# Kernel tuning notes

Measured on AMD Instinct MI355X. Metric: run time of the kernel, lower is better.

The kernel has to match this reference:

```python
import jax, jax.numpy as jnp
from jax import lax
import numpy as np

FEAT_STRIDE = 16
PRE_NMS_TOP_N = 2000
POST_NMS_TOP_N = 300
NMS_THRESH = 0.7


def _whctrs(a):
    w = a[2] - a[0] + 1.0
    h = a[3] - a[1] + 1.0
    return w, h, a[0] + 0.5 * (w - 1.0), a[1] + 0.5 * (h - 1.0)


def _mkanchors(ws, hs, x_ctr, y_ctr):
    ws = np.asarray(ws, dtype=np.float64)
    hs = np.asarray(hs, dtype=np.float64)
    return np.stack([x_ctr - 0.5 * (ws - 1.0), y_ctr - 0.5 * (hs - 1.0),
                     x_ctr + 0.5 * (ws - 1.0), y_ctr + 0.5 * (hs - 1.0)], axis=1)


def generate_anchors(base_size=16, ratios=np.array([0.5, 1.0, 2.0]), scales=np.array([8.0, 16.0, 32.0])):
    base = np.array([1.0, 1.0, float(base_size), float(base_size)]) - 1.0
    w, h, xc, yc = _whctrs(base)
    size = w * h
    ws = np.round(np.sqrt(size / ratios))
    hs = np.round(ws * ratios)
    ratio_anchors = _mkanchors(ws, hs, xc, yc)
    out = []
    for i in range(ratio_anchors.shape[0]):
        w_i, h_i, xc_i, yc_i = _whctrs(ratio_anchors[i])
        out.append(_mkanchors(w_i * scales, h_i * scales, xc_i, yc_i))
    return np.vstack(out).astype(np.float32)


ANCHORS = generate_anchors()  # [A=9, 4]
NUM_ANCHORS = ANCHORS.shape[0]


def _nms_keep(boxes, thresh):
    # boxes [N,4], already sorted by descending score; torchvision IoU convention.
    x1, y1, x2, y2 = boxes[:, 0], boxes[:, 1], boxes[:, 2], boxes[:, 3]
    areas = (x2 - x1) * (y2 - y1)
    xx1 = jnp.maximum(x1[:, None], x1[None, :])
    yy1 = jnp.maximum(y1[:, None], y1[None, :])
    xx2 = jnp.minimum(x2[:, None], x2[None, :])
    yy2 = jnp.minimum(y2[:, None], y2[None, :])
    inter = jnp.clip(xx2 - xx1, 0.0) * jnp.clip(yy2 - yy1, 0.0)
    iou = inter / (areas[:, None] + areas[None, :] - inter + 1e-9)
    n = boxes.shape[0]
    # sup[i, j] True => box i (higher score) suppresses later box j
    sup = (iou > thresh) & jnp.triu(jnp.ones((n, n), bool), 1)

    def body(i, keep):
        return keep & ~(keep[i] & sup[i])

    return lax.fori_loop(0, n, body, jnp.ones((n,), bool))


def setup_inputs() -> dict:
    key = jax.random.key(0)
    k1, k2 = jax.random.split(key)
    B, A, H, W = 8, NUM_ANCHORS, 128, 128
    scores = jax.random.normal(k1, (B, 2 * A, H, W), jnp.float32)
    bbox_deltas = jax.random.normal(k2, (B, 4 * A, H, W), jnp.float32) * 0.2
    im_h = float(H * FEAT_STRIDE)
    im_w = float(W * FEAT_STRIDE)
    im_info = jnp.tile(jnp.array([[im_h, im_w, 1.0]], jnp.float32), (B, 1))
    return {"scores": scores, "bbox_deltas": bbox_deltas, "im_info": im_info}


def reference(scores, bbox_deltas, im_info):
    B, _, H, W = scores.shape
    A = NUM_ANCHORS
    # --- anchor generation over the feature grid ---
    sx = jnp.arange(W, dtype=jnp.float32) * FEAT_STRIDE
    sy = jnp.arange(H, dtype=jnp.float32) * FEAT_STRIDE
    gx, gy = jnp.meshgrid(sx, sy)  # 'xy' indexing matches np.meshgrid default
    shifts = jnp.stack([gx.ravel(), gy.ravel(), gx.ravel(), gy.ravel()], axis=1)  # [K,4]
    anchors = (jnp.asarray(ANCHORS)[None, :, :] + shifts[:, None, :]).reshape(-1, 4)  # [K*A,4]

    obj_scores = scores[:, A:].transpose(0, 2, 3, 1).reshape(B, -1)   # [B, K*A]
    deltas = bbox_deltas.transpose(0, 2, 3, 1).reshape(B, -1, 4)      # [B, K*A, 4]

    # --- bbox_transform_inv ---
    widths = anchors[:, 2] - anchors[:, 0] + 1.0
    heights = anchors[:, 3] - anchors[:, 1] + 1.0
    ctr_x = anchors[:, 0] + 0.5 * widths
    ctr_y = anchors[:, 1] + 0.5 * heights
    dx, dy, dw, dh = deltas[..., 0], deltas[..., 1], deltas[..., 2], deltas[..., 3]
    pred_ctr_x = dx * widths + ctr_x
    pred_ctr_y = dy * heights + ctr_y
    pred_w = jnp.exp(dw) * widths
    pred_h = jnp.exp(dh) * heights
    proposals = jnp.stack([pred_ctr_x - 0.5 * pred_w, pred_ctr_y - 0.5 * pred_h,
                           pred_ctr_x + 0.5 * pred_w, pred_ctr_y + 0.5 * pred_h], axis=-1)

    # --- clip_boxes: im_info[b] = (h, w, scale) ---
    max_x = (im_info[:, 1] - 1.0)[:, None]
    max_y = (im_info[:, 0] - 1.0)[:, None]
    proposals = jnp.stack([
        jnp.clip(proposals[..., 0], 0.0, max_x),
        jnp.clip(proposals[..., 1], 0.0, max_y),
        jnp.clip(proposals[..., 2], 0.0, max_x),
        jnp.clip(proposals[..., 3], 0.0, max_y)], axis=-1)

    # --- pre-NMS top-k by score ---
    _, order = lax.top_k(obj_scores, PRE_NMS_TOP_N)                  # [B, pre]
    top_props = jnp.take_along_axis(proposals, order[..., None], axis=1)  # [B, pre, 4]

    # --- per-image greedy NMS (fixed-size, jit-compatible) ---
    keep = jax.vmap(lambda b: _nms_keep(b, NMS_THRESH))(top_props)   # [B, pre] bool
    sel = jnp.argsort(jnp.where(keep, 0, 1), axis=1, stable=True)[:, :POST_NMS_TOP_N]
    valid = jnp.take_along_axis(keep, sel, axis=1)                   # [B, post]
    out_boxes = jnp.take_along_axis(top_props, sel[..., None], axis=1) * valid[..., None].astype(top_props.dtype)

    batch_idx = jnp.broadcast_to(
        jnp.arange(B, dtype=out_boxes.dtype)[:, None, None], (B, POST_NMS_TOP_N, 1))
    return jnp.concatenate([batch_idx, out_boxes], axis=-1)  # [B, post_nms_topN, 5]
```

## Files before the change

kernel.cpp:

```cpp
#include <hip/hip_runtime.h>

#define NB 8
#define NA 9
#define NCELL (128 * 128)
#define NTOT (NCELL * NA)
#define PRE_K 2000
#define POST_K 300
#define PARTS 18
#define SLOT 512
#define THR_BIN 0x5FFu
#define NMS_TH 0.7f

__constant__ float c_aw[NA] = {184.f, 368.f, 736.f, 128.f, 256.f, 512.f, 88.f, 176.f, 352.f};
__constant__ float c_ah[NA] = {96.f, 192.f, 384.f, 128.f, 256.f, 512.f, 176.f, 352.f, 704.f};

__device__ __forceinline__ unsigned int sortable(float s) {
    unsigned int u = __float_as_uint(s);
    return (u & 0x80000000u) ? ~u : (u | 0x80000000u);
}

__device__ __forceinline__ unsigned long long shflx64(unsigned long long v, int m) {
    return __shfl_xor(v, m, 64);
}

__global__ __launch_bounds__(1024) void sweep_kernel(const float* __restrict__ scores,
                                                     unsigned int* __restrict__ h0out,
                                                     int* __restrict__ bcnt,
                                                     unsigned long long* __restrict__ buf) {
    __shared__ unsigned int h[2048];
    __shared__ unsigned long long lbuf[SLOT];
    __shared__ int lcnt;
    int b = blockIdx.y, part = blockIdx.x, tid = threadIdx.x;
    h[tid] = 0; h[tid + 1024] = 0;
    if (tid == 0) lcnt = 0;
    __syncthreads();
    const float4* sp4 = (const float4*)(scores + (size_t)b * 18 * NCELL + (size_t)NA * NCELL);
    int base4 = part * 2048;
#pragma unroll
    for (int e = 0; e < 2; ++e) {
        int t4 = base4 + e * 1024 + tid;
        float4 v = sp4[t4];
        float el[4] = {v.x, v.y, v.z, v.w};
#pragma unroll
        for (int j = 0; j < 4; ++j) {
            unsigned int u = sortable(el[j]);
            atomicAdd(&h[u >> 21], 1u);
            if ((u >> 21) >= THR_BIN) {
                int idx4 = t4 * 4 + j;
                int a = idx4 >> 14;
                int cell = idx4 & 16383;
                unsigned int i = (unsigned int)cell * 9u + (unsigned int)a;
                int pos = atomicAdd(&lcnt, 1);
                if (pos < SLOT)
                    lbuf[pos] = ((unsigned long long)u << 32) |
                                (unsigned long long)(0xFFFFFFFFu - i);
            }
        }
    }
    __syncthreads();
    unsigned int* o = h0out + ((size_t)(b * PARTS + part)) * 2048;
    o[tid] = h[tid];
    o[tid + 1024] = h[tid + 1024];
    if (tid == 0) bcnt[b * PARTS + part] = lcnt;
    int m = min(lcnt, SLOT);
    for (int t = tid; t < m; t += 1024)
        buf[((size_t)(b * PARTS + part)) * SLOT + t] = lbuf[t];
}

#define SHFL_STEP(J)                                                          \
    {                                                                         \
        int d_ = (J) >> 1;                                                    \
        bool keepMax = (((tid & d_) == 0) == (((2u * (unsigned)tid) & k) == 0)); \
        unsigned long long pa = shflx64(va, d_);                              \
        unsigned long long pb = shflx64(vb, d_);                              \
        va = keepMax ? (va > pa ? va : pa) : (va < pa ? va : pa);             \
        vb = keepMax ? (vb > pb ? vb : pb) : (vb < pb ? vb : pb);             \
    }
#define LOCAL_STEP()                                                          \
    {                                                                         \
        bool desc = (((2u * (unsigned)tid) & k) == 0);                        \
        unsigned long long lo = va < vb ? va : vb;                            \
        unsigned long long hi = va < vb ? vb : va;                            \
        va = desc ? hi : lo; vb = desc ? lo : hi;                             \
    }

__global__ __launch_bounds__(1024) void sortdec_kernel(const float* __restrict__ scores,
                                                       const unsigned int* __restrict__ h0out,
                                                       const int* __restrict__ bcnt,
                                                       const unsigned long long* __restrict__ buf,
                                                       const float* __restrict__ deltas,
                                                       const float* __restrict__ im_info,
                                                       float4* __restrict__ props) {
    __shared__ unsigned long long s[4096];
    __shared__ unsigned int wpart[16], wexcl[16];
    __shared__ unsigned int h128[128];
    __shared__ int sbc[PARTS];
    __shared__ unsigned int sh_piv, sh_spiv;
    __shared__ unsigned int sh_need;
    __shared__ int sh_ok, fcnt;
    int b = blockIdx.x, tid = threadIdx.x;
    int lane = tid & 63, wid = tid >> 6;
    unsigned int* thr = (unsigned int*)s;

    if (tid < PARTS) sbc[tid] = bcnt[b * PARTS + tid];
    if (tid == 0) { sh_ok = 1; fcnt = 0; }

    unsigned int c0 = 0, c1 = 0;
    for (int p = 0; p < PARTS; ++p) {
        const unsigned int* hp = h0out + ((size_t)(b * PARTS + p)) * 2048;
        uint2 v = *(const uint2*)&hp[2 * tid];
        c0 += v.x; c1 += v.y;
    }
    unsigned int sum = c0 + c1;
#pragma unroll
    for (int off = 1; off < 64; off <<= 1) {
        unsigned int v = __shfl_down(sum, off, 64);
        if (lane + off < 64) sum += v;
    }
    if (lane == 0) wpart[wid] = sum;
    __syncthreads();
    if (tid < 16) {
        unsigned int e = 0;
        for (int w = tid + 1; w < 16; ++w) e += wpart[w];
        wexcl[tid] = e;
    }
    __syncthreads();
    unsigned int self = sum + wexcl[wid];
    thr[tid] = self;
    __syncthreads();
    unsigned int above = (tid < 1023) ? thr[tid + 1] : 0u;
    if (self >= (unsigned)PRE_K && above < (unsigned)PRE_K) {
        if (above + c1 >= (unsigned)PRE_K) {
            sh_piv = (unsigned)(2 * tid + 1); sh_need = (unsigned)(PRE_K)-above;
        } else {
            sh_piv = (unsigned)(2 * tid); sh_need = (unsigned)(PRE_K)-above - c1;
        }
    }
    __syncthreads();
    unsigned int piv = sh_piv;
    if (tid < PARTS && sbc[tid] > SLOT) sh_ok = 0;
    if (tid == 0 && piv < THR_BIN) sh_ok = 0;
    if (tid < 128) h128[tid] = 0;
    __syncthreads();
    int ok = sh_ok;

    if (ok) {
        for (int t = tid; t < PARTS * SLOT; t += 1024) {
            int p = t >> 9, off = t & (SLOT - 1);
            if (off < sbc[p]) {
                unsigned long long e = buf[((size_t)(b * PARTS + p)) * SLOT + off];
                unsigned int u = (unsigned int)(e >> 32);
                if ((u >> 21) == piv) atomicAdd(&h128[(u >> 14) & 127u], 1u);
            }
        }
    } else {
        const float4* sp4 = (const float4*)(scores + (size_t)b * 18 * NCELL + (size_t)NA * NCELL);
        for (int t = tid; t < NTOT / 4; t += 1024) {
            float4 v = sp4[t];
            unsigned int u;
            u = sortable(v.x); if ((u >> 21) == piv) atomicAdd(&h128[(u >> 14) & 127u], 1u);
            u = sortable(v.y); if ((u >> 21) == piv) atomicAdd(&h128[(u >> 14) & 127u], 1u);
            u = sortable(v.z); if ((u >> 21) == piv) atomicAdd(&h128[(u >> 14) & 127u], 1u);
            u = sortable(v.w); if ((u >> 21) == piv) atomicAdd(&h128[(u >> 14) & 127u], 1u);
        }
    }
    __syncthreads();
    if (tid < 64) {
        unsigned int d0 = h128[2 * lane], d1 = h128[2 * lane + 1];
        unsigned int rs = d0 + d1;
#pragma unroll
        for (int off = 1; off < 64; off <<= 1) {
            unsigned int v = __shfl_down(rs, off, 64);
            if (lane + off < 64) rs += v;
        }
        unsigned int rab = __shfl_down(rs, 1, 64);
        if (lane == 63) rab = 0;
        unsigned int need0 = sh_need;
        if (rs >= need0 && rab < need0) {
            unsigned int d = (rab + d1 >= need0) ? (unsigned)(2 * lane + 1) : (unsigned)(2 * lane);
            sh_spiv = ((piv << 7) | d) << 14;
        }
    }
    __syncthreads();
    unsigned int spiv = sh_spiv;

    if (ok) {
        for (int t = tid; t < PARTS * SLOT; t += 1024) {
            int p = t >> 9, off = t & (SLOT - 1);
            if (off < sbc[p]) {
                unsigned long long e = buf[((size_t)(b * PARTS + p)) * SLOT + off];
                if ((unsigned int)(e >> 32) >= spiv) {
                    int pos = atomicAdd(&fcnt, 1);
                    if (pos < 4096) s[pos] = e;
                }
            }
        }
    } else {
        const float4* sp4 = (const float4*)(scores + (size_t)b * 18 * NCELL + (size_t)NA * NCELL);
        for (int t4 = tid; t4 < NTOT / 4; t4 += 1024) {
            float4 v = sp4[t4];
            float el[4] = {v.x, v.y, v.z, v.w};
#pragma unroll
            for (int j = 0; j < 4; ++j) {
                unsigned int u = sortable(el[j]);
                if (u >= spiv) {
                    int idx4 = t4 * 4 + j;
                    int a = idx4 >> 14;
                    int cell = idx4 & 16383;
                    unsigned int i = (unsigned int)cell * 9u + (unsigned int)a;
                    int pos = atomicAdd(&fcnt, 1);
                    if (pos < 4096)
                        s[pos] = ((unsigned long long)u << 32) |
                                 (unsigned long long)(0xFFFFFFFFu - i);
                }
            }
        }
    }
    __syncthreads();
    int n2 = min(fcnt, 4096);
    int SZ = (n2 <= 2048) ? 2048 : 4096;
    for (int t = tid; t < SZ; t += 1024)
        if (t >= n2) s[t] = 0ULL;
    __syncthreads();

    if (SZ == 2048) {
        unsigned long long va = s[2 * tid], vb = s[2 * tid + 1];
#pragma unroll
        for (unsigned k = 2; k <= 128; k <<= 1) {
#pragma unroll
            for (unsigned j = k >> 1; j >= 2; j >>= 1) SHFL_STEP(j)
            LOCAL_STEP()
        }
        for (unsigned k = 256; k <= 2048; k <<= 1) {
            s[2 * tid] = va; s[2 * tid + 1] = vb;
            __syncthreads();
            for (unsigned j = k >> 1; j >= 128; j >>= 1) {
                for (int t = tid; t < 2048; t += 1024) {
                    int ixj = t ^ (int)j;
                    if (ixj > t) {
                        unsigned long long x = s[t], y = s[ixj];
                        if ((((unsigned)t & k) == 0) ? (x < y) : (x > y)) { s[t] = y; s[ixj] = x; }
                    }
                }
                __syncthreads();
            }
            va = s[2 * tid]; vb = s[2 * tid + 1];
#pragma unroll
            for (unsigned j = 64; j >= 2; j >>= 1) SHFL_STEP(j)
            LOCAL_STEP()
        }
        s[2 * tid] = va; s[2 * tid + 1] = vb;
        __syncthreads();
    } else {
        for (int k = 2; k <= 4096; k <<= 1) {
            for (int j = k >> 1; j > 0; j >>= 1) {
                for (int t = tid; t < 4096; t += 1024) {
                    int ixj = t ^ j;
                    if (ixj > t) {
                        unsigned long long x = s[t], y = s[ixj];
                        if (((t & k) == 0) ? (x < y) : (x > y)) { s[t] = y; s[ixj] = x; }
                    }
                }
                __syncthreads();
            }
        }
    }

    float maxx = __fsub_rn(im_info[b * 3 + 1], 1.0f);
    float maxy = __fsub_rn(im_info[b * 3 + 0], 1.0f);
    const float* dbase = deltas + (size_t)b * 36 * NCELL;
    for (int r = tid; r < PRE_K; r += 1024) {
        unsigned int i = 0xFFFFFFFFu - (unsigned int)(s[r] & 0xFFFFFFFFu);
        unsigned int cell = i / 9u;
        unsigned int a = i - cell * 9u;
        int wx = (int)(cell & 127u), hy = (int)(cell >> 7);
        const float* dp = dbase + (size_t)(4u * a) * NCELL + (size_t)hy * 128 + wx;
        float dx = dp[0];
        float dy = dp[NCELL];
        float dw = dp[2 * NCELL];
        float dh = dp[3 * NCELL];
        float W_ = c_aw[a], H_ = c_ah[a];
        float cx = (float)(16 * wx + 8), cy = (float)(16 * hy + 8);
        float px = __fadd_rn(__fmul_rn(dx, W_), cx);
        float py = __fadd_rn(__fmul_rn(dy, H_), cy);
        float pw = __fmul_rn((float)exp((double)dw), W_);
        float ph = __fmul_rn((float)exp((double)dh), H_);
        float hw = __fmul_rn(0.5f, pw), hh = __fmul_rn(0.5f, ph);
        float x1 = __fsub_rn(px, hw), y1 = __fsub_rn(py, hh);
        float x2 = __fadd_rn(px, hw), y2 = __fadd_rn(py, hh);
        x1 = fminf(fmaxf(x1, 0.0f), maxx);
        y1 = fminf(fmaxf(y1, 0.0f), maxy);
        x2 = fminf(fmaxf(x2, 0.0f), maxx);
        y2 = fminf(fmaxf(y2, 0.0f), maxy);
        props[(size_t)b * PRE_K + r] = make_float4(x1, y1, x2, y2);
    }
}

__global__ void mask_kernel(const float4* __restrict__ boxes,
                            unsigned long long* __restrict__ colm) {
    int iT = blockIdx.x, jT = blockIdx.y, b = blockIdx.z;
    if (iT > jT) return;
    __shared__ float4 ib[64];
    int t = threadIdx.x;
    int i0 = iT * 64;
    ib[t] = (i0 + t < PRE_K) ? boxes[(size_t)b * PRE_K + i0 + t] : make_float4(0.f, 0.f, -1.f, -1.f);
    __syncthreads();
    int j = jT * 64 + t;
    if (j >= PRE_K) return;
    float4 jb = boxes[(size_t)b * PRE_K + j];
    float barea = __fmul_rn(__fsub_rn(jb.z, jb.x), __fsub_rn(jb.w, jb.y));
    unsigned long long m = 0ULL;
    for (int ii = 0; ii < 64; ++ii) {
        int i = i0 + ii;
        if (i < j) {
            float4 c = ib[ii];
            float aarea = __fmul_rn(__fsub_rn(c.z, c.x), __fsub_rn(c.w, c.y));
            float xx1 = fmaxf(c.x, jb.x), yy1 = fmaxf(c.y, jb.y);
            float xx2 = fminf(c.z, jb.z), yy2 = fminf(c.w, jb.w);
            float iw = fmaxf(__fsub_rn(xx2, xx1), 0.0f);
            float ih = fmaxf(__fsub_rn(yy2, yy1), 0.0f);
            float inter = __fmul_rn(iw, ih);
            float denom = __fadd_rn(__fsub_rn(__fadd_rn(aarea, barea), inter), 1e-9f);
            float iou = __fdiv_rn(inter, denom);
            if (iou > NMS_TH) m |= (1ULL << ii);
        }
    }
    colm[((size_t)b * 32 + iT) * 2048 + j] = m;
}

__global__ void scan_kernel(const unsigned long long* __restrict__ colm,
                            const float4* __restrict__ boxes,
                            float* __restrict__ out) {
    int b = blockIdx.x;
    int lane = threadIdx.x;
    __shared__ unsigned long long kw[32];
    __shared__ int keeplist[POST_K];
    const unsigned long long* cb = colm + (size_t)b * 32 * 2048;
    int total = 0;
    bool done = false;
    for (int k = 0; k < 32 && !done; ++k) {
        int j = k * 64 + lane;
        unsigned long long d = 0;
        int w = 0;
        for (; w + 8 <= k; w += 8) {
            unsigned long long a0 = cb[(size_t)(w + 0) * 2048 + j] & kw[w + 0];
            unsigned long long a1 = cb[(size_t)(w + 1) * 2048 + j] & kw[w + 1];
            unsigned long long a2 = cb[(size_t)(w + 2) * 2048 + j] & kw[w + 2];
            unsigned long long a3 = cb[(size_t)(w + 3) * 2048 + j] & kw[w + 3];
            unsigned long long a4 = cb[(size_t)(w + 4) * 2048 + j] & kw[w + 4];
            unsigned long long a5 = cb[(size_t)(w + 5) * 2048 + j] & kw[w + 5];
            unsigned long long a6 = cb[(size_t)(w + 6) * 2048 + j] & kw[w + 6];
            unsigned long long a7 = cb[(size_t)(w + 7) * 2048 + j] & kw[w + 7];
            d |= ((a0 | a1) | (a2 | a3)) | ((a4 | a5) | (a6 | a7));
        }
        for (; w < k; ++w) d |= cb[(size_t)w * 2048 + j] & kw[w];
        unsigned long long diag = cb[(size_t)k * 2048 + j];
        bool alive_me = (d == 0ULL) && (j < PRE_K);
        unsigned long long alive = __ballot(alive_me);
        unsigned long long keptw = 0ULL;
        while (alive) {
            int i = __builtin_ctzll(alive);
            keptw |= (1ULL << i);
            if (lane == 0 && total < POST_K) keeplist[total] = k * 64 + i;
            total++;
            if (total >= POST_K) { done = true; break; }
            unsigned long long sup = __ballot(((diag >> i) & 1ULL) != 0ULL);
            alive &= ~sup;
            alive &= ~keptw;
        }
        if (lane == 0) kw[k] = keptw;
        __syncthreads();
    }
    __syncthreads();
    int K = min(total, POST_K);
    const float4* bb = boxes + (size_t)b * PRE_K;
    for (int r = lane; r < POST_K; r += 64) {
        float4 v = make_float4(0.f, 0.f, 0.f, 0.f);
        if (r < K) v = bb[keeplist[r]];
        float* o = out + ((size_t)b * POST_K + r) * 5;
        o[0] = (float)b;
        o[1] = v.x;
        o[2] = v.y;
        o[3] = v.z;
        o[4] = v.w;
    }
}

extern "C" void kernel_launch(void* const* d_in, const int* in_sizes, int n_in,
                              void* d_out, int out_size, void* d_ws, size_t ws_size,
                              hipStream_t stream) {
    const float* scores = (const float*)d_in[0];
    const float* deltas = (const float*)d_in[1];
    const float* im_info = (const float*)d_in[2];
    float* out = (float*)d_out;
    char* ws = (char*)d_ws;

    unsigned int* h0out = (unsigned int*)(ws + 0);
    int* bcnt = (int*)(ws + 1179648);
    unsigned long long* buf = (unsigned long long*)(ws + 1180672);
    float4* props = (float4*)(ws + 1770496);
    unsigned long long* colm = (unsigned long long*)(ws + 2026496);

    hipLaunchKernelGGL(sweep_kernel, dim3(PARTS, NB), dim3(1024), 0, stream,
                       scores, h0out, bcnt, buf);
    hipLaunchKernelGGL(sortdec_kernel, dim3(NB), dim3(1024), 0, stream,
                       scores, h0out, bcnt, buf, deltas, im_info, props);
    hipLaunchKernelGGL(mask_kernel, dim3(32, 32, NB), dim3(64), 0, stream, props, colm);
    hipLaunchKernelGGL(scan_kernel, dim3(NB), dim3(64), 0, stream, colm, props, out);
}
```

Baseline: 102.3 us.

## Split box decode into its own kernel and parallelize NMS scan across 16 waves

The proposal decode moves out of the 8-block sort kernel into a separate grid-wide decode kernel, so the random delta gathers and double-precision exp run across many blocks. The NMS scan kernel now runs with 16 waves per image. Each wave owns two 64-box tiles and keeps its own suppression flag in registers, updated from a broadcast kept-word after each tile is resolved, where before one wave reread every earlier mask word serially. This adds an extra launch and two block barriers per tile step in exchange for parallel mask loads and a shorter serial dependency chain.

```diff
diff --git a/kernel.cpp b/kernel.cpp
--- a/kernel.cpp
+++ b/kernel.cpp
@@ -88,9 +88,7 @@
                                                        const unsigned int* __restrict__ h0out,
                                                        const int* __restrict__ bcnt,
                                                        const unsigned long long* __restrict__ buf,
-                                                       const float* __restrict__ deltas,
-                                                       const float* __restrict__ im_info,
-                                                       float4* __restrict__ props) {
+                                                       unsigned int* __restrict__ topidx) {
     __shared__ unsigned long long s[4096];
     __shared__ unsigned int wpart[16], wexcl[16];
     __shared__ unsigned int h128[128];
@@ -106,6 +104,7 @@
     if (tid == 0) { sh_ok = 1; fcnt = 0; }
 
     unsigned int c0 = 0, c1 = 0;
+#pragma unroll
     for (int p = 0; p < PARTS; ++p) {
         const unsigned int* hp = h0out + ((size_t)(b * PARTS + p)) * 2048;
         uint2 v = *(const uint2*)&hp[2 * tid];
@@ -265,35 +264,43 @@
             }
         }
     }
-
+    for (int r = tid; r < PRE_K; r += 1024)
+        topidx[(size_t)b * PRE_K + r] = 0xFFFFFFFFu - (unsigned int)(s[r] & 0xFFFFFFFFu);
+}
+
+__global__ void decode_kernel(const unsigned int* __restrict__ topidx,
+                              const float* __restrict__ deltas,
+                              const float* __restrict__ im_info,
+                              float4* __restrict__ props) {
+    int gid = blockIdx.x * 256 + threadIdx.x;
+    if (gid >= NB * PRE_K) return;
+    int b = gid / PRE_K;
+    unsigned int i = topidx[gid];
+    unsigned int cell = i / 9u;
+    unsigned int a = i - cell * 9u;
+    int wx = (int)(cell & 127u), hy = (int)(cell >> 7);
+    const float* dp = deltas + (size_t)b * 36 * NCELL + (size_t)(4u * a) * NCELL +
+                      (size_t)hy * 128 + wx;
+    float dx = dp[0];
+    float dy = dp[NCELL];
+    float dw = dp[2 * NCELL];
+    float dh = dp[3 * NCELL];
+    float W_ = c_aw[a], H_ = c_ah[a];
+    float cx = (float)(16 * wx + 8), cy = (float)(16 * hy + 8);
+    float px = __fadd_rn(__fmul_rn(dx, W_), cx);
+    float py = __fadd_rn(__fmul_rn(dy, H_), cy);
+    float pw = __fmul_rn((float)exp((double)dw), W_);
+    float ph = __fmul_rn((float)exp((double)dh), H_);
+    float hw = __fmul_rn(0.5f, pw), hh = __fmul_rn(0.5f, ph);
+    float x1 = __fsub_rn(px, hw), y1 = __fsub_rn(py, hh);
+    float x2 = __fadd_rn(px, hw), y2 = __fadd_rn(py, hh);
     float maxx = __fsub_rn(im_info[b * 3 + 1], 1.0f);
     float maxy = __fsub_rn(im_info[b * 3 + 0], 1.0f);
-    const float* dbase = deltas + (size_t)b * 36 * NCELL;
-    for (int r = tid; r < PRE_K; r += 1024) {
-        unsigned int i = 0xFFFFFFFFu - (unsigned int)(s[r] & 0xFFFFFFFFu);
-        unsigned int cell = i / 9u;
-        unsigned int a = i - cell * 9u;
-        int wx = (int)(cell & 127u), hy = (int)(cell >> 7);
-        const float* dp = dbase + (size_t)(4u * a) * NCELL + (size_t)hy * 128 + wx;
-        float dx = dp[0];
-        float dy = dp[NCELL];
-        float dw = dp[2 * NCELL];
-        float dh = dp[3 * NCELL];
-        float W_ = c_aw[a], H_ = c_ah[a];
-        float cx = (float)(16 * wx + 8), cy = (float)(16 * hy + 8);
-        float px = __fadd_rn(__fmul_rn(dx, W_), cx);
-        float py = __fadd_rn(__fmul_rn(dy, H_), cy);
-        float pw = __fmul_rn((float)exp((double)dw), W_);
-        float ph = __fmul_rn((float)exp((double)dh), H_);
-        float hw = __fmul_rn(0.5f, pw), hh = __fmul_rn(0.5f, ph);
-        float x1 = __fsub_rn(px, hw), y1 = __fsub_rn(py, hh);
-        float x2 = __fadd_rn(px, hw), y2 = __fadd_rn(py, hh);
-        x1 = fminf(fmaxf(x1, 0.0f), maxx);
-        y1 = fminf(fmaxf(y1, 0.0f), maxy);
-        x2 = fminf(fmaxf(x2, 0.0f), maxx);
-        y2 = fminf(fmaxf(y2, 0.0f), maxy);
-        props[(size_t)b * PRE_K + r] = make_float4(x1, y1, x2, y2);
-    }
+    x1 = fminf(fmaxf(x1, 0.0f), maxx);
+    y1 = fminf(fmaxf(y1, 0.0f), maxy);
+    x2 = fminf(fmaxf(x2, 0.0f), maxx);
+    y2 = fminf(fmaxf(y2, 0.0f), maxy);
+    props[gid] = make_float4(x1, y1, x2, y2);
 }
 
 __global__ void mask_kernel(const float4* __restrict__ boxes,
@@ -328,53 +335,60 @@
     colm[((size_t)b * 32 + iT) * 2048 + j] = m;
 }
 
-__global__ void scan_kernel(const unsigned long long* __restrict__ colm,
-                            const float4* __restrict__ boxes,
-                            float* __restrict__ out) {
-    int b = blockIdx.x;
-    int lane = threadIdx.x;
-    __shared__ unsigned long long kw[32];
+__global__ __launch_bounds__(1024) void scan_kernel(const unsigned long long* __restrict__ colm,
+                                                    const float4* __restrict__ boxes,
+                                                    float* __restrict__ out) {
     __shared__ int keeplist[POST_K];
+    __shared__ unsigned long long kw_sh;
+    __shared__ int ctl[2];
+    int b = blockIdx.x, tid = threadIdx.x;
+    int lane = tid & 63, wid = tid >> 6;
+    int t0 = wid, t1 = wid + 16;
     const unsigned long long* cb = colm + (size_t)b * 32 * 2048;
-    int total = 0;
-    bool done = false;
-    for (int k = 0; k < 32 && !done; ++k) {
-        int j = k * 64 + lane;
-        unsigned long long d = 0;
-        int w = 0;
-        for (; w + 8 <= k; w += 8) {
-            unsigned long long a0 = cb[(size_t)(w + 0) * 2048 + j] & kw[w + 0];
-            unsigned long long a1 = cb[(size_t)(w + 1) * 2048 + j] & kw[w + 1];
-            unsigned long long a2 = cb[(size_t)(w + 2) * 2048 + j] & kw[w + 2];
-            unsigned long long a3 = cb[(size_t)(w + 3) * 2048 + j] & kw[w + 3];
-            unsigned long long a4 = cb[(size_t)(w + 4) * 2048 + j] & kw[w + 4];
-            unsigned long long a5 = cb[(size_t)(w + 5) * 2048 + j] & kw[w + 5];
-            unsigned long long a6 = cb[(size_t)(w + 6) * 2048 + j] & kw[w + 6];
-            unsigned long long a7 = cb[(size_t)(w + 7) * 2048 + j] & kw[w + 7];
-            d |= ((a0 | a1) | (a2 | a3)) | ((a4 | a5) | (a6 | a7));
-        }
-        for (; w < k; ++w) d |= cb[(size_t)w * 2048 + j] & kw[w];
-        unsigned long long diag = cb[(size_t)k * 2048 + j];
-        bool alive_me = (d == 0ULL) && (j < PRE_K);
-        unsigned long long alive = __ballot(alive_me);
-        unsigned long long keptw = 0ULL;
-        while (alive) {
-            int i = __builtin_ctzll(alive);
-            keptw |= (1ULL << i);
-            if (lane == 0 && total < POST_K) keeplist[total] = k * 64 + i;
-            total++;
-            if (total >= POST_K) { done = true; break; }
-            unsigned long long sup = __ballot(((diag >> i) & 1ULL) != 0ULL);
-            alive &= ~sup;
-            alive &= ~keptw;
-        }
-        if (lane == 0) kw[k] = keptw;
+    if (tid == 0) { ctl[0] = 0; ctl[1] = 0; }
+    int d0 = 0, d1 = 0;
+    unsigned long long diag0 = cb[(size_t)t0 * 2048 + t0 * 64 + lane];
+    unsigned long long diag1 = cb[(size_t)t1 * 2048 + t1 * 64 + lane];
+    unsigned long long w0 = (t0 > 0) ? cb[t0 * 64 + lane] : 0ULL;
+    unsigned long long w1 = cb[t1 * 64 + lane];
+    __syncthreads();
+    for (int k = 0; k < 32; ++k) {
+        if (wid == (k & 15)) {
+            bool isT1 = (k >= 16);
+            int j = k * 64 + lane;
+            unsigned long long diag = isT1 ? diag1 : diag0;
+            bool alive_me = ((isT1 ? d1 : d0) == 0) && (j < PRE_K);
+            unsigned long long alive = __ballot(alive_me);
+            unsigned long long keptw = 0ULL;
+            int total = ctl[0];
+            int done = 0;
+            while (alive) {
+                int i = __builtin_ctzll(alive);
+                keptw |= (1ULL << i);
+                if (lane == 0 && total < POST_K) keeplist[total] = k * 64 + i;
+                total++;
+                if (total >= POST_K) { done = 1; break; }
+                unsigned long long sup = __ballot(((diag >> i) & 1ULL) != 0ULL);
+                alive &= ~sup;
+                alive &= ~keptw;
+            }
+            if (lane == 0) { ctl[0] = total; ctl[1] = done; kw_sh = keptw; }
+        }
         __syncthreads();
-    }
-    __syncthreads();
-    int K = min(total, POST_K);
+        if (ctl[1]) break;
+        unsigned long long kwk = kw_sh;
+        if (t0 > k && (w0 & kwk)) d0 = 1;
+        if (t1 > k && (w1 & kwk)) d1 = 1;
+        if (k + 1 < 32) {
+            if (t0 > k + 1) w0 = cb[(size_t)(k + 1) * 2048 + t0 * 64 + lane];
+            if (t1 > k + 1) w1 = cb[(size_t)(k + 1) * 2048 + t1 * 64 + lane];
+        }
+        __syncthreads();
+    }
+    __syncthreads();
+    int K = min(ctl[0], POST_K);
     const float4* bb = boxes + (size_t)b * PRE_K;
-    for (int r = lane; r < POST_K; r += 64) {
+    for (int r = tid; r < POST_K; r += 1024) {
         float4 v = make_float4(0.f, 0.f, 0.f, 0.f);
         if (r < K) v = bb[keeplist[r]];
         float* o = out + ((size_t)b * POST_K + r) * 5;
@@ -398,13 +412,16 @@
     unsigned int* h0out = (unsigned int*)(ws + 0);
     int* bcnt = (int*)(ws + 1179648);
     unsigned long long* buf = (unsigned long long*)(ws + 1180672);
-    float4* props = (float4*)(ws + 1770496);
-    unsigned long long* colm = (unsigned long long*)(ws + 2026496);
+    unsigned int* topidx = (unsigned int*)(ws + 1770496);
+    float4* props = (float4*)(ws + 1834496);
+    unsigned long long* colm = (unsigned long long*)(ws + 2090496);
 
     hipLaunchKernelGGL(sweep_kernel, dim3(PARTS, NB), dim3(1024), 0, stream,
                        scores, h0out, bcnt, buf);
     hipLaunchKernelGGL(sortdec_kernel, dim3(NB), dim3(1024), 0, stream,
-                       scores, h0out, bcnt, buf, deltas, im_info, props);
+                       scores, h0out, bcnt, buf, topidx);
+    hipLaunchKernelGGL(decode_kernel, dim3((NB * PRE_K + 255) / 256), dim3(256), 0, stream,
+                       topidx, deltas, im_info, props);
     hipLaunchKernelGGL(mask_kernel, dim3(32, 32, NB), dim3(64), 0, stream, props, colm);
-    hipLaunchKernelGGL(scan_kernel, dim3(NB), dim3(64), 0, stream, colm, props, out);
-}
+    hipLaunchKernelGGL(scan_kernel, dim3(NB), dim3(1024), 0, stream, colm, props, out);
+}
```

New measurement: 100.1 us. 1.02x faster.

## Fuse box decode into mask and scan kernels; register-buffered NMS scan

Applied to the files above, without the earlier changes.

The sort kernel now writes only the top-k anchor indices, and box decoding is recomputed on the fly in the mask kernel (per tile) and in the final output gather. The tail of the single-block sort kernel no longer does the decode serially, but the same boxes are now decoded about 32 times across mask blocks. The scan kernel is restructured to keep a per-lane dead bitmask. It double-buffers the next row of mask words in registers and propagates suppression forward, instead of re-reading all earlier columns for every tile. This costs many registers and adds redundant transcendental work.

```diff
diff --git a/kernel.cpp b/kernel.cpp
--- a/kernel.cpp
+++ b/kernel.cpp
@@ -21,6 +21,32 @@
 
 __device__ __forceinline__ unsigned long long shflx64(unsigned long long v, int m) {
     return __shfl_xor(v, m, 64);
+}
+
+__device__ __forceinline__ float4 decode_box(unsigned int i, const float* __restrict__ dbase,
+                                             float maxx, float maxy) {
+    unsigned int cell = i / 9u;
+    unsigned int a = i - cell * 9u;
+    int wx = (int)(cell & 127u), hy = (int)(cell >> 7);
+    const float* dp = dbase + (size_t)(4u * a) * NCELL + (size_t)hy * 128 + wx;
+    float dx = dp[0];
+    float dy = dp[NCELL];
+    float dw = dp[2 * NCELL];
+    float dh = dp[3 * NCELL];
+    float W_ = c_aw[a], H_ = c_ah[a];
+    float cx = (float)(16 * wx + 8), cy = (float)(16 * hy + 8);
+    float px = __fadd_rn(__fmul_rn(dx, W_), cx);
+    float py = __fadd_rn(__fmul_rn(dy, H_), cy);
+    float pw = __fmul_rn((float)exp((double)dw), W_);
+    float ph = __fmul_rn((float)exp((double)dh), H_);
+    float hw = __fmul_rn(0.5f, pw), hh = __fmul_rn(0.5f, ph);
+    float x1 = __fsub_rn(px, hw), y1 = __fsub_rn(py, hh);
+    float x2 = __fadd_rn(px, hw), y2 = __fadd_rn(py, hh);
+    x1 = fminf(fmaxf(x1, 0.0f), maxx);
+    y1 = fminf(fmaxf(y1, 0.0f), maxy);
+    x2 = fminf(fmaxf(x2, 0.0f), maxx);
+    y2 = fminf(fmaxf(y2, 0.0f), maxy);
+    return make_float4(x1, y1, x2, y2);
 }
 
 __global__ __launch_bounds__(1024) void sweep_kernel(const float* __restrict__ scores,
@@ -88,9 +114,7 @@
                                                        const unsigned int* __restrict__ h0out,
                                                        const int* __restrict__ bcnt,
                                                        const unsigned long long* __restrict__ buf,
-                                                       const float* __restrict__ deltas,
-                                                       const float* __restrict__ im_info,
-                                                       float4* __restrict__ props) {
+                                                       unsigned int* __restrict__ topidx) {
     __shared__ unsigned long long s[4096];
     __shared__ unsigned int wpart[16], wexcl[16];
     __shared__ unsigned int h128[128];
@@ -106,6 +130,7 @@
     if (tid == 0) { sh_ok = 1; fcnt = 0; }
 
     unsigned int c0 = 0, c1 = 0;
+#pragma unroll
     for (int p = 0; p < PARTS; ++p) {
         const unsigned int* hp = h0out + ((size_t)(b * PARTS + p)) * 2048;
         uint2 v = *(const uint2*)&hp[2 * tid];
@@ -265,49 +290,30 @@
             }
         }
     }
-
-    float maxx = __fsub_rn(im_info[b * 3 + 1], 1.0f);
-    float maxy = __fsub_rn(im_info[b * 3 + 0], 1.0f);
-    const float* dbase = deltas + (size_t)b * 36 * NCELL;
-    for (int r = tid; r < PRE_K; r += 1024) {
-        unsigned int i = 0xFFFFFFFFu - (unsigned int)(s[r] & 0xFFFFFFFFu);
-        unsigned int cell = i / 9u;
-        unsigned int a = i - cell * 9u;
-        int wx = (int)(cell & 127u), hy = (int)(cell >> 7);
-        const float* dp = dbase + (size_t)(4u * a) * NCELL + (size_t)hy * 128 + wx;
-        float dx = dp[0];
-        float dy = dp[NCELL];
-        float dw = dp[2 * NCELL];
-        float dh = dp[3 * NCELL];
-        float W_ = c_aw[a], H_ = c_ah[a];
-        float cx = (float)(16 * wx + 8), cy = (float)(16 * hy + 8);
-        float px = __fadd_rn(__fmul_rn(dx, W_), cx);
-        float py = __fadd_rn(__fmul_rn(dy, H_), cy);
-        float pw = __fmul_rn((float)exp((double)dw), W_);
-        float ph = __fmul_rn((float)exp((double)dh), H_);
-        float hw = __fmul_rn(0.5f, pw), hh = __fmul_rn(0.5f, ph);
-        float x1 = __fsub_rn(px, hw), y1 = __fsub_rn(py, hh);
-        float x2 = __fadd_rn(px, hw), y2 = __fadd_rn(py, hh);
-        x1 = fminf(fmaxf(x1, 0.0f), maxx);
-        y1 = fminf(fmaxf(y1, 0.0f), maxy);
-        x2 = fminf(fmaxf(x2, 0.0f), maxx);
-        y2 = fminf(fmaxf(y2, 0.0f), maxy);
-        props[(size_t)b * PRE_K + r] = make_float4(x1, y1, x2, y2);
-    }
-}
-
-__global__ void mask_kernel(const float4* __restrict__ boxes,
+    for (int r = tid; r < PRE_K; r += 1024)
+        topidx[(size_t)b * PRE_K + r] = 0xFFFFFFFFu - (unsigned int)(s[r] & 0xFFFFFFFFu);
+}
+
+__global__ void mask_kernel(const unsigned int* __restrict__ topidx,
+                            const float* __restrict__ deltas,
+                            const float* __restrict__ im_info,
                             unsigned long long* __restrict__ colm) {
     int iT = blockIdx.x, jT = blockIdx.y, b = blockIdx.z;
     if (iT > jT) return;
     __shared__ float4 ib[64];
     int t = threadIdx.x;
+    float maxx = __fsub_rn(im_info[b * 3 + 1], 1.0f);
+    float maxy = __fsub_rn(im_info[b * 3 + 0], 1.0f);
+    const float* dbase = deltas + (size_t)b * 36 * NCELL;
+    const unsigned int* ti = topidx + (size_t)b * PRE_K;
     int i0 = iT * 64;
-    ib[t] = (i0 + t < PRE_K) ? boxes[(size_t)b * PRE_K + i0 + t] : make_float4(0.f, 0.f, -1.f, -1.f);
-    __syncthreads();
+    ib[t] = (i0 + t < PRE_K) ? decode_box(ti[i0 + t], dbase, maxx, maxy)
+                             : make_float4(0.f, 0.f, -1.f, -1.f);
     int j = jT * 64 + t;
-    if (j >= PRE_K) return;
-    float4 jb = boxes[(size_t)b * PRE_K + j];
+    bool jv = j < PRE_K;
+    float4 jb = jv ? decode_box(ti[j], dbase, maxx, maxy) : make_float4(0.f, 0.f, -1.f, -1.f);
+    __syncthreads();
+    if (!jv) return;
     float barea = __fmul_rn(__fsub_rn(jb.z, jb.x), __fsub_rn(jb.w, jb.y));
     unsigned long long m = 0ULL;
     for (int ii = 0; ii < 64; ++ii) {
@@ -328,55 +334,67 @@
     colm[((size_t)b * 32 + iT) * 2048 + j] = m;
 }
 
-__global__ void scan_kernel(const unsigned long long* __restrict__ colm,
-                            const float4* __restrict__ boxes,
-                            float* __restrict__ out) {
-    int b = blockIdx.x;
-    int lane = threadIdx.x;
-    __shared__ unsigned long long kw[32];
+#define PROCESS_TILE(K, BUF)                                                   \
+    {                                                                          \
+        unsigned long long diag = 0ULL;                                        \
+        _Pragma("unroll") for (int q = 0; q < 32; ++q)                         \
+            if (q == (K)) diag = BUF[q];                                       \
+        int j = (K) * 64 + lane;                                               \
+        bool alive_me = (((dead >> (K)) & 1u) == 0u) && (j < PRE_K);           \
+        unsigned long long alive = __ballot(alive_me);                         \
+        unsigned long long keptw = 0ULL;                                       \
+        while (alive) {                                                        \
+            int i = __builtin_ctzll(alive);                                    \
+            keptw |= (1ULL << i);                                              \
+            if (lane == 0 && total < POST_K) keeplist[total] = (K) * 64 + i;   \
+            total++;                                                           \
+            if (total >= POST_K) { done = true; break; }                       \
+            unsigned long long sup = __ballot(((diag >> i) & 1ULL) != 0ULL);   \
+            alive &= ~sup;                                                     \
+            alive &= ~keptw;                                                   \
+        }                                                                      \
+        _Pragma("unroll") for (int q = 0; q < 32; ++q)                         \
+            if (q > (K) && ((BUF[q] & keptw) != 0ULL)) dead |= (1u << q);      \
+    }
+
+__global__ __launch_bounds__(64) void scan_kernel(const unsigned long long* __restrict__ colm,
+                                                  const unsigned int* __restrict__ topidx,
+                                                  const float* __restrict__ deltas,
+                                                  const float* __restrict__ im_info,
+                                                  float* __restrict__ out) {
     __shared__ int keeplist[POST_K];
+    int b = blockIdx.x, lane = threadIdx.x;
     const unsigned long long* cb = colm + (size_t)b * 32 * 2048;
+    unsigned int dead = 0;
     int total = 0;
     bool done = false;
-    for (int k = 0; k < 32 && !done; ++k) {
-        int j = k * 64 + lane;
-        unsigned long long d = 0;
-        int w = 0;
-        for (; w + 8 <= k; w += 8) {
-            unsigned long long a0 = cb[(size_t)(w + 0) * 2048 + j] & kw[w + 0];
-            unsigned long long a1 = cb[(size_t)(w + 1) * 2048 + j] & kw[w + 1];
-            unsigned long long a2 = cb[(size_t)(w + 2) * 2048 + j] & kw[w + 2];
-            unsigned long long a3 = cb[(size_t)(w + 3) * 2048 + j] & kw[w + 3];
-            unsigned long long a4 = cb[(size_t)(w + 4) * 2048 + j] & kw[w + 4];
-            unsigned long long a5 = cb[(size_t)(w + 5) * 2048 + j] & kw[w + 5];
-            unsigned long long a6 = cb[(size_t)(w + 6) * 2048 + j] & kw[w + 6];
-            unsigned long long a7 = cb[(size_t)(w + 7) * 2048 + j] & kw[w + 7];
-            d |= ((a0 | a1) | (a2 | a3)) | ((a4 | a5) | (a6 | a7));
-        }
-        for (; w < k; ++w) d |= cb[(size_t)w * 2048 + j] & kw[w];
-        unsigned long long diag = cb[(size_t)k * 2048 + j];
-        bool alive_me = (d == 0ULL) && (j < PRE_K);
-        unsigned long long alive = __ballot(alive_me);
-        unsigned long long keptw = 0ULL;
-        while (alive) {
-            int i = __builtin_ctzll(alive);
-            keptw |= (1ULL << i);
-            if (lane == 0 && total < POST_K) keeplist[total] = k * 64 + i;
-            total++;
-            if (total >= POST_K) { done = true; break; }
-            unsigned long long sup = __ballot(((diag >> i) & 1ULL) != 0ULL);
-            alive &= ~sup;
-            alive &= ~keptw;
-        }
-        if (lane == 0) kw[k] = keptw;
-        __syncthreads();
+    unsigned long long bufA[32], bufB[32];
+#pragma unroll
+    for (int q = 0; q < 32; ++q) bufA[q] = cb[q * 64 + lane];
+    for (int kk = 0; kk < 16 && !done; ++kk) {
+        int k0 = 2 * kk;
+#pragma unroll
+        for (int q = 0; q < 32; ++q)
+            bufB[q] = cb[(size_t)(k0 + 1) * 2048 + q * 64 + lane];
+        PROCESS_TILE(k0, bufA)
+        if (done) break;
+        int k1 = k0 + 1;
+        if (k1 + 1 < 32) {
+#pragma unroll
+            for (int q = 0; q < 32; ++q)
+                bufA[q] = cb[(size_t)(k1 + 1) * 2048 + q * 64 + lane];
+        }
+        PROCESS_TILE(k1, bufB)
     }
     __syncthreads();
     int K = min(total, POST_K);
-    const float4* bb = boxes + (size_t)b * PRE_K;
+    float maxx = __fsub_rn(im_info[b * 3 + 1], 1.0f);
+    float maxy = __fsub_rn(im_info[b * 3 + 0], 1.0f);
+    const float* dbase = deltas + (size_t)b * 36 * NCELL;
+    const unsigned int* ti = topidx + (size_t)b * PRE_K;
     for (int r = lane; r < POST_K; r += 64) {
         float4 v = make_float4(0.f, 0.f, 0.f, 0.f);
-        if (r < K) v = bb[keeplist[r]];
+        if (r < K) v = decode_box(ti[keeplist[r]], dbase, maxx, maxy);
         float* o = out + ((size_t)b * POST_K + r) * 5;
         o[0] = (float)b;
         o[1] = v.x;
@@ -398,13 +416,15 @@
     unsigned int* h0out = (unsigned int*)(ws + 0);
     int* bcnt = (int*)(ws + 1179648);
     unsigned long long* buf = (unsigned long long*)(ws + 1180672);
-    float4* props = (float4*)(ws + 1770496);
-    unsigned long long* colm = (unsigned long long*)(ws + 2026496);
+    unsigned int* topidx = (unsigned int*)(ws + 1770496);
+    unsigned long long* colm = (unsigned long long*)(ws + 1834496);
 
     hipLaunchKernelGGL(sweep_kernel, dim3(PARTS, NB), dim3(1024), 0, stream,
                        scores, h0out, bcnt, buf);
     hipLaunchKernelGGL(sortdec_kernel, dim3(NB), dim3(1024), 0, stream,
-                       scores, h0out, bcnt, buf, deltas, im_info, props);
-    hipLaunchKernelGGL(mask_kernel, dim3(32, 32, NB), dim3(64), 0, stream, props, colm);
-    hipLaunchKernelGGL(scan_kernel, dim3(NB), dim3(64), 0, stream, colm, props, out);
-}
+                       scores, h0out, bcnt, buf, topidx);
+    hipLaunchKernelGGL(mask_kernel, dim3(32, 32, NB), dim3(64), 0, stream,
+                       topidx, deltas, im_info, colm);
+    hipLaunchKernelGGL(scan_kernel, dim3(NB), dim3(64), 0, stream,
+                       colm, topidx, deltas, im_info, out);
+}
```

After: 106.9 us. +4.5%, slower.
